# Kernel tuning notes

Measured on AMD Instinct MI355X. Metric: run time of the kernel, lower is better.

## Reference

```python
import jax, jax.numpy as jnp
import numpy as np

N = 4_194_304
NUM_ITER = 6
DAMPING = 0.95
TOL = 1e-06
EPS = 1e-12


def _translate_x(dx):
    """4x4 homogeneous translation along the optical (x) axis."""
    return jnp.eye(4, dtype=dx.dtype).at[0, 3].set(dx)


def setup_inputs() -> dict:
    key = jax.random.key(0)
    k1, k2, k3 = jax.random.split(key, 3)
    # Ray origins: near x = -10, transverse spread within/around the aperture
    px = -10.0 + 0.5 * jax.random.normal(k1, (N, 1), dtype=jnp.float32)
    pyz = 8.0 * jax.random.normal(k2, (N, 2), dtype=jnp.float32)
    P = jnp.concatenate([px, pyz], axis=-1)
    # Ray directions: mostly +x, small transverse components, normalized
    vyz = 0.05 * jax.random.normal(k3, (N, 2), dtype=jnp.float32)
    V = jnp.concatenate([jnp.ones((N, 1), jnp.float32), vyz], axis=-1)
    V = V / jnp.linalg.norm(V, axis=-1, keepdims=True)
    tf = jnp.eye(4, dtype=jnp.float32)
    return {
        "P": P,
        "V": V,
        "tf": tf,
        "diameter": jnp.float32(50.0),
        "C": jnp.float32(0.02),
        "anchors": jnp.zeros((2,), jnp.float32),
        "scale": jnp.float32(1.0),
        "normalize": jnp.asarray(False),
    }


def reference(P, V, tf, diameter, C, anchors, scale, normalize):
    # normalize: curvature interpreted relative to semi-diameter
    C_eff = jnp.where(normalize, C * 2.0 / diameter, C)
    s2 = scale * scale

    def sag(r2):  # scaled spherical sag: f = scale * g(r2/scale^2)
        u = r2 / s2
        root = jnp.sqrt(jnp.clip(1.0 - C_eff * C_eff * u, EPS))
        return scale * C_eff * u / (1.0 + root)

    def sag_grad(y, z):  # (df/dy, df/dz) = C*(y,z) / (scale*sqrt(1-C^2 u))
        u = (y * y + z * z) / s2
        root = jnp.sqrt(jnp.clip(1.0 - C_eff * C_eff * u, EPS))
        k = C_eff / (scale * root)
        return k * y, k * z

    # anchors shift the surface along x by fractions of the edge sag (extent)
    extent = sag(jnp.square(diameter * 0.5))
    surface_tf = tf @ _translate_x(-anchors[0] * extent)
    next_tf = tf @ _translate_x((anchors[1] - anchors[0]) * extent)

    # Rays into surface-local frame
    R = surface_tf[:3, :3]
    tv = surface_tf[:3, 3]
    Pl = (P - tv) @ R  # [N,3] = R^T (P - t)
    Vl = V @ R
    vx, vy, vz = Vl[:, 0], Vl[:, 1], Vl[:, 2]

    safe_vx = jnp.where(jnp.abs(vx) > EPS, vx, EPS)
    t = -Pl[:, 0] / safe_vx  # init: intersection with plane x=0

    # Damped Newton on F(t) = sag(y(t),z(t)) - x(t)
    for _ in range(NUM_ITER):
        p = Pl + t[:, None] * Vl
        y, z = p[:, 1], p[:, 2]
        F = sag(y * y + z * z) - p[:, 0]
        gy, gz = sag_grad(y, z)
        dF = gy * vy + gz * vz - vx
        dF = jnp.where(jnp.abs(dF) > EPS, dF, EPS)
        t = t - DAMPING * F / dF

    p = Pl + t[:, None] * Vl
    y, z = p[:, 1], p[:, 2]
    r2 = y * y + z * z
    F = sag(r2) - p[:, 0]
    gy, gz = sag_grad(y, z)
    # implicit-surface normal: grad(sag(y,z) - x) = (-1, gy, gz), normalized
    n_local = jnp.stack([-jnp.ones_like(gy), gy, gz], axis=-1)
    n_local = n_local / jnp.linalg.norm(n_local, axis=-1, keepdims=True)
    normals = n_local @ R.T  # back to global frame

    valid = (r2 <= jnp.square(diameter * 0.5)) & (jnp.abs(F) < 100.0 * TOL)
    return t, normals, valid, surface_tf, next_tf
```

## Files before the change

kernel.cpp:

```cpp
#include <hip/hip_runtime.h>

#define F_EPS 1e-12f
#define F_DAMPING 0.95f
#define N_ITER 6
#define TPB 256

__launch_bounds__(TPB)
__global__ void trace_kernel(const float* __restrict__ P,
                             const float* __restrict__ V,
                             const float* __restrict__ tf,
                             const float* __restrict__ diameter,
                             const float* __restrict__ Cc,
                             const float* __restrict__ anchors,
                             const float* __restrict__ scale_p,
                             const unsigned char* __restrict__ normalize,
                             float* __restrict__ out,
                             int n)
{
    __shared__ float4 sbuf[TPB * 3];
    const int tid  = threadIdx.x;
    const int base = (blockIdx.x * TPB + tid) * 4;

    float R0,R1,R2,R3,R4,R5,R6,R7,R8, tv0,tv1,tv2;
    float C_eff, scale, half_d2, inv_s2;
    {
#pragma clang fp contract(off)
        float d  = diameter[0];
        float c  = Cc[0];
        float sc = scale_p[0];
        bool  nrm = (normalize[0] != 0);
        C_eff = nrm ? (c * 2.0f / d) : c;
        float s2 = sc * sc;
        float hr = d * 0.5f;
        half_d2 = hr * hr;
        float u = half_d2 / s2;
        float root = sqrtf(fmaxf(1.0f - (C_eff * C_eff) * u, F_EPS));
        float extent = sc * C_eff * u / (1.0f + root);
        float a0 = anchors[0], a1 = anchors[1];
        float dx0 = -a0 * extent;
        float dx1 = (a1 - a0) * extent;
        R0 = tf[0]; R1 = tf[1]; R2 = tf[2];
        R3 = tf[4]; R4 = tf[5]; R5 = tf[6];
        R6 = tf[8]; R7 = tf[9]; R8 = tf[10];
        tv0 = tf[0] * dx0 + tf[3];
        tv1 = tf[4] * dx0 + tf[7];
        tv2 = tf[8] * dx0 + tf[11];
        scale  = sc;
        inv_s2 = 1.0f / s2;
        if (blockIdx.x == 0 && tid < 16) {
            int i = tid >> 2, j = tid & 3;
            float v  = tf[tid];
            float sv = (j == 3) ? (tf[i * 4] * dx0 + v) : v;
            float nv = (j == 3) ? (tf[i * 4] * dx1 + v) : v;
            float* out_tail = out + (size_t)n * 5;
            out_tail[tid]      = sv;
            out_tail[16 + tid] = nv;
        }
    }
    float ce2   = C_eff * C_eff;
    float sC    = scale * C_eff;
    float a_num = sC * inv_s2;
    float ce2s  = ce2 * inv_s2;
    float Cs    = C_eff / scale;

    const bool full_block = ((blockIdx.x + 1) * (TPB * 4) <= n);

    float Px[4], Py[4], Pz[4], Vx[4], Vy[4], Vz[4];
    if (full_block) {
        const size_t bf4 = (size_t)blockIdx.x * (TPB * 3);
        const float4* P4 = reinterpret_cast<const float4*>(P);
        const float4* V4 = reinterpret_cast<const float4*>(V);
        float4 p0 = P4[bf4 + tid], p1 = P4[bf4 + TPB + tid], p2 = P4[bf4 + 2*TPB + tid];
        float4 q0 = V4[bf4 + tid], q1 = V4[bf4 + TPB + tid], q2 = V4[bf4 + 2*TPB + tid];
        sbuf[tid] = p0; sbuf[TPB + tid] = p1; sbuf[2*TPB + tid] = p2;
        __syncthreads();
        float4 a = sbuf[3*tid], b = sbuf[3*tid + 1], c = sbuf[3*tid + 2];
        __syncthreads();
        Px[0]=a.x; Py[0]=a.y; Pz[0]=a.z; Px[1]=a.w; Py[1]=b.x; Pz[1]=b.y;
        Px[2]=b.z; Py[2]=b.w; Pz[2]=c.x; Px[3]=c.y; Py[3]=c.z; Pz[3]=c.w;
        sbuf[tid] = q0; sbuf[TPB + tid] = q1; sbuf[2*TPB + tid] = q2;
        __syncthreads();
        a = sbuf[3*tid]; b = sbuf[3*tid + 1]; c = sbuf[3*tid + 2];
        __syncthreads();
        Vx[0]=a.x; Vy[0]=a.y; Vz[0]=a.z; Vx[1]=a.w; Vy[1]=b.x; Vz[1]=b.y;
        Vx[2]=b.z; Vy[2]=b.w; Vz[2]=c.x; Vx[3]=c.y; Vy[3]=c.z; Vz[3]=c.w;
    } else {
        for (int r = 0; r < 4; ++r) {
            int i = base + r;
            if (i < n) {
                Px[r] = P[(size_t)i*3 + 0]; Py[r] = P[(size_t)i*3 + 1]; Pz[r] = P[(size_t)i*3 + 2];
                Vx[r] = V[(size_t)i*3 + 0]; Vy[r] = V[(size_t)i*3 + 1]; Vz[r] = V[(size_t)i*3 + 2];
            } else {
                Px[r] = 0.0f; Py[r] = 0.0f; Pz[r] = 0.0f;
                Vx[r] = 1.0f; Vy[r] = 0.0f; Vz[r] = 0.0f;
            }
        }
    }

    float Plx[4], Ply[4], Plz[4], vx[4], vy[4], vz[4], tN[4];
#pragma unroll
    for (int r = 0; r < 4; ++r) {
        float px0 = Px[r] - tv0, py0 = Py[r] - tv1, pz0 = Pz[r] - tv2;
        Plx[r] = px0 * R0 + py0 * R3 + pz0 * R6;
        Ply[r] = px0 * R1 + py0 * R4 + pz0 * R7;
        Plz[r] = px0 * R2 + py0 * R5 + pz0 * R8;
        vx[r] = Vx[r] * R0 + Vy[r] * R3 + Vz[r] * R6;
        vy[r] = Vx[r] * R1 + Vy[r] * R4 + Vz[r] * R7;
        vz[r] = Vx[r] * R2 + Vy[r] * R5 + Vz[r] * R8;
        float safe_vx = (fabsf(vx[r]) > F_EPS) ? vx[r] : F_EPS;
        tN[r] = (-Plx[r]) * __builtin_amdgcn_rcpf(safe_vx);
    }

#pragma unroll
    for (int it = 0; it < N_ITER; ++it) {
#pragma unroll
        for (int r = 0; r < 4; ++r) {
            float pxx = fmaf(tN[r], vx[r], Plx[r]);
            float py  = fmaf(tN[r], vy[r], Ply[r]);
            float pz  = fmaf(tN[r], vz[r], Plz[r]);
            float r2  = fmaf(py, py, pz * pz);
            float m   = fmaxf(fmaf(-ce2s, r2, 1.0f), F_EPS);
            float rsq = __builtin_amdgcn_rsqf(m);
            float root = m * rsq;
            float k    = Cs * rsq;
            float ird  = __builtin_amdgcn_rcpf(1.0f + root);
            float F    = fmaf(a_num * r2, ird, -pxx);
            float dF = fmaf(k * py, vy[r], fmaf(k * pz, vz[r], -vx[r]));
            dF = (fabsf(dF) > F_EPS) ? dF : F_EPS;
            tN[r] = fmaf(-F_DAMPING * F, __builtin_amdgcn_rcpf(dF), tN[r]);
        }
    }

    float tres[4], nxo[4], nyo[4], nzo[4], val[4];
#pragma unroll
    for (int r = 0; r < 4; ++r) {
        float pxx = fmaf(tN[r], vx[r], Plx[r]);
        float py  = fmaf(tN[r], vy[r], Ply[r]);
        float pz  = fmaf(tN[r], vz[r], Plz[r]);
        float r2  = fmaf(py, py, pz * pz);
        float m   = fmaxf(fmaf(-ce2s, r2, 1.0f), F_EPS);
        float rsq = __builtin_amdgcn_rsqf(m);
        float root = m * rsq;
        float k    = Cs * rsq;
        float ird  = __builtin_amdgcn_rcpf(1.0f + root);
        float F    = fmaf(a_num * r2, ird, -pxx);
        float gy = k * py, gz = k * pz;
        float nn2 = fmaf(gy, gy, fmaf(gz, gz, 1.0f));
        float irn = __builtin_amdgcn_rsqf(nn2);
        float nlx = -irn, nly = gy * irn, nlz = gz * irn;
        nxo[r] = nlx * R0 + nly * R1 + nlz * R2;
        nyo[r] = nlx * R3 + nly * R4 + nlz * R5;
        nzo[r] = nlx * R6 + nly * R7 + nlz * R8;
        tres[r] = tN[r];
        val[r]  = ((r2 <= half_d2) && (fabsf(F) < 1e-4f)) ? 1.0f : 0.0f;
    }

    float* t_out = out;
    float* n_out = out + (size_t)n;
    float* v_out = out + (size_t)n * 4;
    if (full_block) {
        sbuf[3*tid]     = make_float4(nxo[0], nyo[0], nzo[0], nxo[1]);
        sbuf[3*tid + 1] = make_float4(nyo[1], nzo[1], nxo[2], nyo[2]);
        sbuf[3*tid + 2] = make_float4(nzo[2], nxo[3], nyo[3], nzo[3]);
        __syncthreads();
        const size_t bf4 = (size_t)blockIdx.x * (TPB * 3);
        float4* N4 = reinterpret_cast<float4*>(n_out);
        N4[bf4 + tid]         = sbuf[tid];
        N4[bf4 + TPB + tid]   = sbuf[TPB + tid];
        N4[bf4 + 2*TPB + tid] = sbuf[2*TPB + tid];
        *reinterpret_cast<float4*>(t_out + base) = make_float4(tres[0], tres[1], tres[2], tres[3]);
        *reinterpret_cast<float4*>(v_out + base) = make_float4(val[0], val[1], val[2], val[3]);
    } else {
        for (int r = 0; r < 4; ++r) {
            int i = base + r;
            if (i < n) {
                t_out[i] = tres[r];
                n_out[(size_t)i*3 + 0] = nxo[r];
                n_out[(size_t)i*3 + 1] = nyo[r];
                n_out[(size_t)i*3 + 2] = nzo[r];
                v_out[i] = val[r];
            }
        }
    }
}

extern "C" void kernel_launch(void* const* d_in, const int* in_sizes, int n_in,
                              void* d_out, int out_size, void* d_ws, size_t ws_size,
                              hipStream_t stream) {
    const float* P  = (const float*)d_in[0];
    const float* V  = (const float*)d_in[1];
    const float* tf = (const float*)d_in[2];
    const float* diameter = (const float*)d_in[3];
    const float* C  = (const float*)d_in[4];
    const float* anchors = (const float*)d_in[5];
    const float* scale = (const float*)d_in[6];
    const unsigned char* normalize = (const unsigned char*)d_in[7];
    int n = in_sizes[0] / 3;
    float* out = (float*)d_out;

    int rays_per_block = TPB * 4;
    int blocks = (n + rays_per_block - 1) / rays_per_block;
    trace_kernel<<<blocks, TPB, 0, stream>>>(P, V, tf, diameter, C, anchors, scale,
                                             normalize, out, n);
}
```

Measured before the change: 177.8 us.

## Process four tiles per block with register double-buffered loads, drop LDS transpose

Each block now handles four consecutive tiles of 1024 rays, prefetching the next tile's P/V float4s into registers while computing the current one. The shared-memory transpose and its barriers are removed: each thread reads three contiguous float4s directly, which gives strided rather than fully coalesced accesses. The aim is to overlap load latency with compute and cut block count and sync overhead. The cost is higher register pressure, fewer blocks, and possibly less efficient memory transactions.

```diff
diff --git a/kernel.cpp b/kernel.cpp
--- a/kernel.cpp
+++ b/kernel.cpp
@@ -4,6 +4,9 @@
 #define F_DAMPING 0.95f
 #define N_ITER 6
 #define TPB 256
+#define RPT 4
+#define TILE (TPB * RPT)
+#define TILES 4
 
 __launch_bounds__(TPB)
 __global__ void trace_kernel(const float* __restrict__ P,
@@ -17,9 +20,7 @@
                              float* __restrict__ out,
                              int n)
 {
-    __shared__ float4 sbuf[TPB * 3];
-    const int tid  = threadIdx.x;
-    const int base = (blockIdx.x * TPB + tid) * 4;
+    const int tid = threadIdx.x;
 
     float R0,R1,R2,R3,R4,R5,R6,R7,R8, tv0,tv1,tv2;
     float C_eff, scale, half_d2, inv_s2;
@@ -57,62 +58,66 @@
             out_tail[16 + tid] = nv;
         }
     }
-    float ce2   = C_eff * C_eff;
-    float sC    = scale * C_eff;
-    float a_num = sC * inv_s2;
-    float ce2s  = ce2 * inv_s2;
-    float Cs    = C_eff / scale;
-
-    const bool full_block = ((blockIdx.x + 1) * (TPB * 4) <= n);
-
-    float Px[4], Py[4], Pz[4], Vx[4], Vy[4], Vz[4];
-    if (full_block) {
-        const size_t bf4 = (size_t)blockIdx.x * (TPB * 3);
-        const float4* P4 = reinterpret_cast<const float4*>(P);
-        const float4* V4 = reinterpret_cast<const float4*>(V);
-        float4 p0 = P4[bf4 + tid], p1 = P4[bf4 + TPB + tid], p2 = P4[bf4 + 2*TPB + tid];
-        float4 q0 = V4[bf4 + tid], q1 = V4[bf4 + TPB + tid], q2 = V4[bf4 + 2*TPB + tid];
-        sbuf[tid] = p0; sbuf[TPB + tid] = p1; sbuf[2*TPB + tid] = p2;
-        __syncthreads();
-        float4 a = sbuf[3*tid], b = sbuf[3*tid + 1], c = sbuf[3*tid + 2];
-        __syncthreads();
-        Px[0]=a.x; Py[0]=a.y; Pz[0]=a.z; Px[1]=a.w; Py[1]=b.x; Pz[1]=b.y;
-        Px[2]=b.z; Py[2]=b.w; Pz[2]=c.x; Px[3]=c.y; Py[3]=c.z; Pz[3]=c.w;
-        sbuf[tid] = q0; sbuf[TPB + tid] = q1; sbuf[2*TPB + tid] = q2;
-        __syncthreads();
-        a = sbuf[3*tid]; b = sbuf[3*tid + 1]; c = sbuf[3*tid + 2];
-        __syncthreads();
-        Vx[0]=a.x; Vy[0]=a.y; Vz[0]=a.z; Vx[1]=a.w; Vy[1]=b.x; Vz[1]=b.y;
-        Vx[2]=b.z; Vy[2]=b.w; Vz[2]=c.x; Vx[3]=c.y; Vy[3]=c.z; Vz[3]=c.w;
-    } else {
+    const float ce2   = C_eff * C_eff;
+    const float sC    = scale * C_eff;
+    const float a_num = sC * inv_s2;
+    const float ce2s  = ce2 * inv_s2;
+    const float Cs    = C_eff / scale;
+
+    float* t_out = out;
+    float* n_out = out + (size_t)n;
+    float* v_out = out + (size_t)n * 4;
+
+    const float4* P4 = reinterpret_cast<const float4*>(P);
+    const float4* V4 = reinterpret_cast<const float4*>(V);
+    float4*       N4 = reinterpret_cast<float4*>(n_out);
+
+    const int total_full = n / TILE;
+    const int tile0 = blockIdx.x * TILES;
+
+    auto process = [&](float4 p0, float4 p1, float4 p2,
+                       float4 q0, float4 q1, float4 q2, int tile) {
+        float Px[4], Py[4], Pz[4], Vx[4], Vy[4], Vz[4];
+        Px[0]=p0.x; Py[0]=p0.y; Pz[0]=p0.z; Px[1]=p0.w; Py[1]=p1.x; Pz[1]=p1.y;
+        Px[2]=p1.z; Py[2]=p1.w; Pz[2]=p2.x; Px[3]=p2.y; Py[3]=p2.z; Pz[3]=p2.w;
+        Vx[0]=q0.x; Vy[0]=q0.y; Vz[0]=q0.z; Vx[1]=q0.w; Vy[1]=q1.x; Vz[1]=q1.y;
+        Vx[2]=q1.z; Vy[2]=q1.w; Vz[2]=q2.x; Vx[3]=q2.y; Vy[3]=q2.z; Vz[3]=q2.w;
+
+        float Plx[4], Ply[4], Plz[4], vx[4], vy[4], vz[4], tN[4];
+#pragma unroll
         for (int r = 0; r < 4; ++r) {
-            int i = base + r;
-            if (i < n) {
-                Px[r] = P[(size_t)i*3 + 0]; Py[r] = P[(size_t)i*3 + 1]; Pz[r] = P[(size_t)i*3 + 2];
-                Vx[r] = V[(size_t)i*3 + 0]; Vy[r] = V[(size_t)i*3 + 1]; Vz[r] = V[(size_t)i*3 + 2];
-            } else {
-                Px[r] = 0.0f; Py[r] = 0.0f; Pz[r] = 0.0f;
-                Vx[r] = 1.0f; Vy[r] = 0.0f; Vz[r] = 0.0f;
+            float px0 = Px[r] - tv0, py0 = Py[r] - tv1, pz0 = Pz[r] - tv2;
+            Plx[r] = px0 * R0 + py0 * R3 + pz0 * R6;
+            Ply[r] = px0 * R1 + py0 * R4 + pz0 * R7;
+            Plz[r] = px0 * R2 + py0 * R5 + pz0 * R8;
+            vx[r] = Vx[r] * R0 + Vy[r] * R3 + Vz[r] * R6;
+            vy[r] = Vx[r] * R1 + Vy[r] * R4 + Vz[r] * R7;
+            vz[r] = Vx[r] * R2 + Vy[r] * R5 + Vz[r] * R8;
+            float safe_vx = (fabsf(vx[r]) > F_EPS) ? vx[r] : F_EPS;
+            tN[r] = (-Plx[r]) * __builtin_amdgcn_rcpf(safe_vx);
+        }
+
+#pragma unroll
+        for (int it = 0; it < N_ITER; ++it) {
+#pragma unroll
+            for (int r = 0; r < 4; ++r) {
+                float pxx = fmaf(tN[r], vx[r], Plx[r]);
+                float py  = fmaf(tN[r], vy[r], Ply[r]);
+                float pz  = fmaf(tN[r], vz[r], Plz[r]);
+                float r2  = fmaf(py, py, pz * pz);
+                float m   = fmaxf(fmaf(-ce2s, r2, 1.0f), F_EPS);
+                float rsq = __builtin_amdgcn_rsqf(m);
+                float root = m * rsq;
+                float k    = Cs * rsq;
+                float ird  = __builtin_amdgcn_rcpf(1.0f + root);
+                float F    = fmaf(a_num * r2, ird, -pxx);
+                float dF = fmaf(k * py, vy[r], fmaf(k * pz, vz[r], -vx[r]));
+                dF = (fabsf(dF) > F_EPS) ? dF : F_EPS;
+                tN[r] = fmaf(-F_DAMPING * F, __builtin_amdgcn_rcpf(dF), tN[r]);
             }
         }
-    }
-
-    float Plx[4], Ply[4], Plz[4], vx[4], vy[4], vz[4], tN[4];
-#pragma unroll
-    for (int r = 0; r < 4; ++r) {
-        float px0 = Px[r] - tv0, py0 = Py[r] - tv1, pz0 = Pz[r] - tv2;
-        Plx[r] = px0 * R0 + py0 * R3 + pz0 * R6;
-        Ply[r] = px0 * R1 + py0 * R4 + pz0 * R7;
-        Plz[r] = px0 * R2 + py0 * R5 + pz0 * R8;
-        vx[r] = Vx[r] * R0 + Vy[r] * R3 + Vz[r] * R6;
-        vy[r] = Vx[r] * R1 + Vy[r] * R4 + Vz[r] * R7;
-        vz[r] = Vx[r] * R2 + Vy[r] * R5 + Vz[r] * R8;
-        float safe_vx = (fabsf(vx[r]) > F_EPS) ? vx[r] : F_EPS;
-        tN[r] = (-Plx[r]) * __builtin_amdgcn_rcpf(safe_vx);
-    }
-
-#pragma unroll
-    for (int it = 0; it < N_ITER; ++it) {
+
+        float tres[4], nxo[4], nyo[4], nzo[4], val[4];
 #pragma unroll
         for (int r = 0; r < 4; ++r) {
             float pxx = fmaf(tN[r], vx[r], Plx[r]);
@@ -125,61 +130,102 @@
             float k    = Cs * rsq;
             float ird  = __builtin_amdgcn_rcpf(1.0f + root);
             float F    = fmaf(a_num * r2, ird, -pxx);
-            float dF = fmaf(k * py, vy[r], fmaf(k * pz, vz[r], -vx[r]));
-            dF = (fabsf(dF) > F_EPS) ? dF : F_EPS;
-            tN[r] = fmaf(-F_DAMPING * F, __builtin_amdgcn_rcpf(dF), tN[r]);
-        }
-    }
-
-    float tres[4], nxo[4], nyo[4], nzo[4], val[4];
-#pragma unroll
-    for (int r = 0; r < 4; ++r) {
-        float pxx = fmaf(tN[r], vx[r], Plx[r]);
-        float py  = fmaf(tN[r], vy[r], Ply[r]);
-        float pz  = fmaf(tN[r], vz[r], Plz[r]);
-        float r2  = fmaf(py, py, pz * pz);
-        float m   = fmaxf(fmaf(-ce2s, r2, 1.0f), F_EPS);
-        float rsq = __builtin_amdgcn_rsqf(m);
-        float root = m * rsq;
-        float k    = Cs * rsq;
-        float ird  = __builtin_amdgcn_rcpf(1.0f + root);
-        float F    = fmaf(a_num * r2, ird, -pxx);
-        float gy = k * py, gz = k * pz;
-        float nn2 = fmaf(gy, gy, fmaf(gz, gz, 1.0f));
-        float irn = __builtin_amdgcn_rsqf(nn2);
-        float nlx = -irn, nly = gy * irn, nlz = gz * irn;
-        nxo[r] = nlx * R0 + nly * R1 + nlz * R2;
-        nyo[r] = nlx * R3 + nly * R4 + nlz * R5;
-        nzo[r] = nlx * R6 + nly * R7 + nlz * R8;
-        tres[r] = tN[r];
-        val[r]  = ((r2 <= half_d2) && (fabsf(F) < 1e-4f)) ? 1.0f : 0.0f;
-    }
-
-    float* t_out = out;
-    float* n_out = out + (size_t)n;
-    float* v_out = out + (size_t)n * 4;
-    if (full_block) {
-        sbuf[3*tid]     = make_float4(nxo[0], nyo[0], nzo[0], nxo[1]);
-        sbuf[3*tid + 1] = make_float4(nyo[1], nzo[1], nxo[2], nyo[2]);
-        sbuf[3*tid + 2] = make_float4(nzo[2], nxo[3], nyo[3], nzo[3]);
-        __syncthreads();
-        const size_t bf4 = (size_t)blockIdx.x * (TPB * 3);
-        float4* N4 = reinterpret_cast<float4*>(n_out);
-        N4[bf4 + tid]         = sbuf[tid];
-        N4[bf4 + TPB + tid]   = sbuf[TPB + tid];
-        N4[bf4 + 2*TPB + tid] = sbuf[2*TPB + tid];
+            float gy = k * py, gz = k * pz;
+            float nn2 = fmaf(gy, gy, fmaf(gz, gz, 1.0f));
+            float irn = __builtin_amdgcn_rsqf(nn2);
+            float nlx = -irn, nly = gy * irn, nlz = gz * irn;
+            nxo[r] = nlx * R0 + nly * R1 + nlz * R2;
+            nyo[r] = nlx * R3 + nly * R4 + nlz * R5;
+            nzo[r] = nlx * R6 + nly * R7 + nlz * R8;
+            tres[r] = tN[r];
+            val[r]  = ((r2 <= half_d2) && (fabsf(F) < 1e-4f)) ? 1.0f : 0.0f;
+        }
+
+        int base = tile * TILE + 4 * tid;
         *reinterpret_cast<float4*>(t_out + base) = make_float4(tres[0], tres[1], tres[2], tres[3]);
         *reinterpret_cast<float4*>(v_out + base) = make_float4(val[0], val[1], val[2], val[3]);
-    } else {
-        for (int r = 0; r < 4; ++r) {
-            int i = base + r;
-            if (i < n) {
-                t_out[i] = tres[r];
-                n_out[(size_t)i*3 + 0] = nxo[r];
-                n_out[(size_t)i*3 + 1] = nyo[r];
-                n_out[(size_t)i*3 + 2] = nzo[r];
-                v_out[i] = val[r];
+        size_t f4 = (size_t)tile * (TILE * 3 / 4) + 3 * tid;
+        N4[f4]     = make_float4(nxo[0], nyo[0], nzo[0], nxo[1]);
+        N4[f4 + 1] = make_float4(nyo[1], nzo[1], nxo[2], nyo[2]);
+        N4[f4 + 2] = make_float4(nzo[2], nxo[3], nyo[3], nzo[3]);
+    };
+
+    float4 c0, c1, c2, c3, c4, c5;
+    float4 x0, x1, x2, x3, x4, x5;
+
+#define LOADT(T, a0, a1, a2, b0, b1, b2)                         \
+    do {                                                         \
+        size_t f4_ = (size_t)(T) * (TILE * 3 / 4) + 3 * tid;     \
+        a0 = P4[f4_]; a1 = P4[f4_ + 1]; a2 = P4[f4_ + 2];        \
+        b0 = V4[f4_]; b1 = V4[f4_ + 1]; b2 = V4[f4_ + 2];        \
+    } while (0)
+
+    if (tile0 < total_full) {
+        LOADT(tile0, c0, c1, c2, c3, c4, c5);
+#pragma unroll
+        for (int k = 0; k < TILES; ++k) {
+            int tile = tile0 + k;
+            if (tile >= total_full) break;
+            bool have_next = (k + 1 < TILES) && (tile + 1 < total_full);
+            if (have_next) LOADT(tile + 1, x0, x1, x2, x3, x4, x5);
+            process(c0, c1, c2, c3, c4, c5, tile);
+            if (have_next) { c0 = x0; c1 = x1; c2 = x2; c3 = x3; c4 = x4; c5 = x5; }
+        }
+    }
+#undef LOADT
+
+    const int rem = n - total_full * TILE;
+    if (rem > 0 && total_full >= tile0 && total_full < tile0 + TILES) {
+        const int start = total_full * TILE;
+        for (int r = 0; r < RPT; ++r) {
+            int i = start + tid * RPT + r;
+            if (i >= n) break;
+            float Pxs = P[(size_t)i * 3 + 0], Pys = P[(size_t)i * 3 + 1], Pzs = P[(size_t)i * 3 + 2];
+            float Vxs = V[(size_t)i * 3 + 0], Vys = V[(size_t)i * 3 + 1], Vzs = V[(size_t)i * 3 + 2];
+            float px0 = Pxs - tv0, py0 = Pys - tv1, pz0 = Pzs - tv2;
+            float Plx = px0 * R0 + py0 * R3 + pz0 * R6;
+            float Ply = px0 * R1 + py0 * R4 + pz0 * R7;
+            float Plz = px0 * R2 + py0 * R5 + pz0 * R8;
+            float vx = Vxs * R0 + Vys * R3 + Vzs * R6;
+            float vy = Vxs * R1 + Vys * R4 + Vzs * R7;
+            float vz = Vxs * R2 + Vys * R5 + Vzs * R8;
+            float safe_vx = (fabsf(vx) > F_EPS) ? vx : F_EPS;
+            float tN = (-Plx) * __builtin_amdgcn_rcpf(safe_vx);
+#pragma unroll
+            for (int it = 0; it < N_ITER; ++it) {
+                float pxx = fmaf(tN, vx, Plx);
+                float py  = fmaf(tN, vy, Ply);
+                float pz  = fmaf(tN, vz, Plz);
+                float r2  = fmaf(py, py, pz * pz);
+                float m   = fmaxf(fmaf(-ce2s, r2, 1.0f), F_EPS);
+                float rsq = __builtin_amdgcn_rsqf(m);
+                float root = m * rsq;
+                float k    = Cs * rsq;
+                float ird  = __builtin_amdgcn_rcpf(1.0f + root);
+                float F    = fmaf(a_num * r2, ird, -pxx);
+                float dF = fmaf(k * py, vy, fmaf(k * pz, vz, -vx));
+                dF = (fabsf(dF) > F_EPS) ? dF : F_EPS;
+                tN = fmaf(-F_DAMPING * F, __builtin_amdgcn_rcpf(dF), tN);
             }
+            float pxx = fmaf(tN, vx, Plx);
+            float py  = fmaf(tN, vy, Ply);
+            float pz  = fmaf(tN, vz, Plz);
+            float r2  = fmaf(py, py, pz * pz);
+            float m   = fmaxf(fmaf(-ce2s, r2, 1.0f), F_EPS);
+            float rsq = __builtin_amdgcn_rsqf(m);
+            float root = m * rsq;
+            float k    = Cs * rsq;
+            float ird  = __builtin_amdgcn_rcpf(1.0f + root);
+            float F    = fmaf(a_num * r2, ird, -pxx);
+            float gy = k * py, gz = k * pz;
+            float nn2 = fmaf(gy, gy, fmaf(gz, gz, 1.0f));
+            float irn = __builtin_amdgcn_rsqf(nn2);
+            float nlx = -irn, nly = gy * irn, nlz = gz * irn;
+            t_out[i] = tN;
+            n_out[(size_t)i * 3 + 0] = nlx * R0 + nly * R1 + nlz * R2;
+            n_out[(size_t)i * 3 + 1] = nlx * R3 + nly * R4 + nlz * R5;
+            n_out[(size_t)i * 3 + 2] = nlx * R6 + nly * R7 + nlz * R8;
+            v_out[i] = ((r2 <= half_d2) && (fabsf(F) < 1e-4f)) ? 1.0f : 0.0f;
         }
     }
 }
@@ -198,8 +244,9 @@
     int n = in_sizes[0] / 3;
     float* out = (float*)d_out;
 
-    int rays_per_block = TPB * 4;
-    int blocks = (n + rays_per_block - 1) / rays_per_block;
+    int total_tiles = (n + TILE - 1) / TILE;
+    int blocks = (total_tiles + TILES - 1) / TILES;
+    if (blocks < 1) blocks = 1;
     trace_kernel<<<blocks, TPB, 0, stream>>>(P, V, tf, diameter, C, anchors, scale,
                                              normalize, out, n);
 }
```

After: 179.0 us. No clear change (+0.7%).
